# Kernel optimization log

Hardware: AMD Instinct MI355X
Metric: run time of the kernel (lower is better)

The kernel has to match this reference:

```python
import jax, jax.numpy as jnp
import numpy as np

DIM = 768
NUM_HEADS = 12
HEAD_DIM = DIM // NUM_HEADS
SCALE = HEAD_DIM ** -0.5


def setup_inputs() -> dict:
    key = jax.random.key(0)
    ks = jax.random.split(key, 8)
    B, Nx, Ny = 4, 1024, 2048
    std = DIM ** -0.5
    return {
        "x": jax.random.normal(ks[0], (B, Nx, DIM), dtype=jnp.float32),
        "y": jax.random.normal(ks[1], (B, Ny, DIM), dtype=jnp.float32),
        "Wq": jax.random.normal(ks[2], (DIM, DIM), dtype=jnp.float32) * std,
        "Wk": jax.random.normal(ks[3], (DIM, DIM), dtype=jnp.float32) * std,
        "Wv": jax.random.normal(ks[4], (DIM, DIM), dtype=jnp.float32) * std,
        "Wproj": jax.random.normal(ks[5], (DIM, DIM), dtype=jnp.float32) * std,
        "bproj": jnp.zeros((DIM,), dtype=jnp.float32),
    }


def reference(x, y, Wq, Wk, Wv, Wproj, bproj):
    B, Nx, C = x.shape
    Ny = y.shape[1]
    H, D = NUM_HEADS, HEAD_DIM
    # Linear projections (torch nn.Linear: x @ W.T), then split heads -> [B,H,N,D]
    q = (x @ Wq.T).reshape(B, Nx, H, D).transpose(0, 2, 1, 3)
    k = (y @ Wk.T).reshape(B, Ny, H, D).transpose(0, 2, 1, 3)
    v = (y @ Wv.T).reshape(B, Ny, H, D).transpose(0, 2, 1, 3)
    # Manual attention: full [B,H,Nx,Ny] score matrix (faithful to source)
    attn = jnp.einsum("bhqd,bhkd->bhqk", q, k) * SCALE
    attn = jax.nn.softmax(attn, axis=-1)
    out = jnp.einsum("bhqk,bhkd->bhqd", attn, v)
    out = out.transpose(0, 2, 1, 3).reshape(B, Nx, C)
    return out @ Wproj.T + bproj
```

## Files before the change

kernel.cpp:

```cpp
#include <hip/hip_runtime.h>
#include <hip/hip_bf16.h>

typedef unsigned short u16;
typedef __attribute__((ext_vector_type(8))) short bf16x8;
typedef __attribute__((ext_vector_type(4))) float f32x4;
typedef __attribute__((ext_vector_type(16))) float f32x16;
typedef __attribute__((ext_vector_type(4))) unsigned u32x4;

#define MFMA(a, b, c) __builtin_amdgcn_mfma_f32_16x16x32_bf16(a, b, c, 0, 0, 0)
#define MFMA32(a, b, c) __builtin_amdgcn_mfma_f32_32x32x16_bf16(a, b, c, 0, 0, 0)

#define STAGE16(g, l) __builtin_amdgcn_global_load_lds( \
    (const __attribute__((address_space(1))) void*)(g),  \
    (__attribute__((address_space(3))) void*)(l), 16, 0, 0)

#define EXP2(x) __builtin_amdgcn_exp2f(x)

__device__ __forceinline__ u16 f2bf(float f) {
  union { float f; unsigned u; } v; v.f = f;
  return (u16)((v.u + 0x7fffu + ((v.u >> 16) & 1u)) >> 16);
}

__device__ __forceinline__ unsigned pack_bf2(float lo, float hi) {
  unsigned r;
  asm("v_cvt_pk_bf16_f32 %0, %1, %2" : "=v"(r) : "v"(lo), "v"(hi));
  return r;
}

__device__ __forceinline__ void pl32swap(unsigned &a, unsigned &b) {
  asm("v_permlane32_swap_b32 %0, %1" : "+v"(a), "+v"(b));
}

__global__ __launch_bounds__(256) void convert_all(
    const float* __restrict__ x, const float* __restrict__ y,
    const float* __restrict__ wq, const float* __restrict__ wk,
    const float* __restrict__ wv, const float* __restrict__ wp,
    u16* __restrict__ xb, u16* __restrict__ yb,
    u16* __restrict__ wqb, u16* __restrict__ wkb,
    u16* __restrict__ wvb, u16* __restrict__ wpb)
{
  constexpr int G0 = 4096 * 768 / 4;
  constexpr int G1 = G0 + 8192 * 768 / 4;
  constexpr int GW = 768 * 768 / 4;
  int g = blockIdx.x * 256 + threadIdx.x;
  const float* s; u16* d; int o;
  if      (g < G0)          { s = x;  d = xb;  o = g; }
  else if (g < G1)          { s = y;  d = yb;  o = g - G0; }
  else if (g < G1 + GW)     { s = wq; d = wqb; o = g - G1; }
  else if (g < G1 + 2*GW)   { s = wk; d = wkb; o = g - G1 - GW; }
  else if (g < G1 + 3*GW)   { s = wv; d = wvb; o = g - G1 - 2*GW; }
  else if (g < G1 + 4*GW)   { s = wp; d = wpb; o = g - G1 - 3*GW; }
  else return;
  float4 v = reinterpret_cast<const float4*>(s)[o];
  ushort4 r;
  r.x = f2bf(v.x); r.y = f2bf(v.y); r.z = f2bf(v.z); r.w = f2bf(v.w);
  reinterpret_cast<ushort4*>(d)[o] = r;
}

template <bool PROJ>
__global__ __launch_bounds__(256) void gemm_k(
    const u16* __restrict__ A0, const u16* __restrict__ A1,
    const u16* __restrict__ W0, const u16* __restrict__ W1,
    const u16* __restrict__ W2,
    u16* __restrict__ Qa, u16* __restrict__ Ka, u16* __restrict__ Vw,
    const float* __restrict__ bias, float* __restrict__ fout)
{
  __shared__ u16 sA[128 * 64];
  __shared__ u16 sB[128 * 64];

  const int nper = PROJ ? 24 : 120;
  int bid = (blockIdx.x & 7) * nper + (blockIdx.x >> 3);

  const u16 *A, *W;
  int mode, mt, nt;
  if (PROJ)           { mode = 3; A = A0; W = W0; mt = bid / 6;        nt = bid % 6; }
  else if (bid < 192) { mode = 0; A = A0; W = W0; mt = bid / 6;        nt = bid % 6; }
  else if (bid < 576) { mode = 1; A = A1; W = W1; mt = (bid-192) / 6;  nt = (bid-192) % 6; }
  else                { mode = 2; A = A1; W = W2; mt = (bid-576) / 6;  nt = (bid-576) % 6; }

  const int tid = threadIdx.x;
  const int w = tid >> 6, l = tid & 63;
  const int wm = w >> 1, wn = w & 1;
  const int g = l >> 4, m = l & 15;

  const int mbase = mt * 128, nbase = nt * 128;

  const int srow = l >> 3;
  const int schunk = ((l & 7) ^ srow) * 8;
  const u16* Ag = A + (size_t)(mbase + srow) * 768 + schunk;
  const u16* Wg = W + (size_t)(nbase + srow) * 768 + schunk;

  f32x4 acc[4][4] = {};

  for (int kt = 0; kt < 12; ++kt) {
    __syncthreads();
    const int ko = kt * 64;
#pragma unroll
    for (int i = 0; i < 4; ++i) {
      const int ri = (i * 4 + w) * 8;
      STAGE16(Ag + (size_t)ri * 768 + ko, (char*)sA + ri * 128);
      STAGE16(Wg + (size_t)ri * 768 + ko, (char*)sB + ri * 128);
    }
    __syncthreads();

    bf16x8 af[2][4], bfr[2][4];
#pragma unroll
    for (int c = 0; c < 2; ++c)
#pragma unroll
      for (int t = 0; t < 4; ++t) {
        const int ar = wm * 64 + t * 16 + m;
        const int br = wn * 64 + t * 16 + m;
        const int cp = ((c * 4 + g) ^ (l & 7)) * 16;
        af[c][t]  = *reinterpret_cast<const bf16x8*>((const char*)sA + ar * 128 + cp);
        bfr[c][t] = *reinterpret_cast<const bf16x8*>((const char*)sB + br * 128 + cp);
      }
#pragma unroll
    for (int c = 0; c < 2; ++c)
#pragma unroll
      for (int mi = 0; mi < 4; ++mi)
#pragma unroll
        for (int ni = 0; ni < 4; ++ni)
          acc[mi][ni] = MFMA(af[c][mi], bfr[c][ni], acc[mi][ni]);
  }

  const float QSCALE = 0.18033688011112042f;
  const int rowb = mbase + wm * 64 + g * 4;
  const int colb = nbase + wn * 64 + m;
#pragma unroll
  for (int mi = 0; mi < 4; ++mi) {
#pragma unroll
    for (int ni = 0; ni < 4; ++ni) {
      const int col = colb + ni * 16;
      const int h = col >> 6, d = col & 63;
      const int t_ = d >> 4, hh = (d >> 3) & 1, di = d & 7;
      const int fo = t_ * 512 + hh * 256 + di;
      if constexpr (PROJ) {
#pragma unroll
        for (int r = 0; r < 4; ++r) {
          const int row = rowb + mi * 16 + r;
          fout[(size_t)row * 768 + col] = acc[mi][ni][r] + bias[col];
        }
      } else {
        if (mode == 0) {
#pragma unroll
          for (int r = 0; r < 4; ++r) {
            const int row = rowb + mi * 16 + r;
            const int b_ = row >> 10, n = row & 1023;
            Qa[((size_t)(b_ * 12 + h) * 32 + (n >> 5)) * 2048 + fo + (n & 31) * 8] =
                f2bf(acc[mi][ni][r] * QSCALE);
          }
        } else if (mode == 1) {
#pragma unroll
          for (int r = 0; r < 4; ++r) {
            const int row = rowb + mi * 16 + r;
            const int b_ = row >> 11, n = row & 2047;
            Ka[(size_t)(b_ * 12 + h) * 131072 + (n >> 5) * 2048 + fo + (n & 31) * 8] =
                f2bf(acc[mi][ni][r]);
          }
        } else {
          const int row = rowb + mi * 16;
          const int b_ = row >> 11, n = row & 2047;
          ushort4 pk;
          pk.x = f2bf(acc[mi][ni][0]); pk.y = f2bf(acc[mi][ni][1]);
          pk.z = f2bf(acc[mi][ni][2]); pk.w = f2bf(acc[mi][ni][3]);
          *reinterpret_cast<ushort4*>(
              Vw + (size_t)(b_ * 12 + h) * 131072 + (n >> 3) * 512 + d * 8 + (n & 7)) = pk;
        }
      }
    }
  }
}

__global__ __launch_bounds__(128, 3) void attn_fwd(
    const u16* __restrict__ Qa, const u16* __restrict__ Ka,
    const u16* __restrict__ Vw, u16* __restrict__ AOb)
{
  __shared__ float cO[32 * 64];
  __shared__ float cL[32];

  const int bid = blockIdx.x;
  const int bh = bid % 48, qt = bid / 48;
  const int tid = threadIdx.x;
  const int w = tid >> 6, l = tid & 63;
  const int h = l >> 5, q = l & 31;

  const u16* qb = Qa + (size_t)(bh * 32 + qt) * 2048 + h * 256 + q * 8;
  bf16x8 qf[4];
#pragma unroll
  for (int t = 0; t < 4; ++t)
    qf[t] = *reinterpret_cast<const bf16x8*>(qb + t * 512);

  const u16* kb = Ka + (size_t)bh * 131072 + (size_t)w * 65536 + h * 256 + q * 8;
  const u16* vb = Vw + (size_t)bh * 131072 + (size_t)w * 65536 + h * 512 + q * 8;

  bf16x8 ones;
#pragma unroll
  for (int i = 0; i < 8; ++i) ones[i] = (short)0x3F80;

  f32x16 o0 = {}, o1 = {}, la = {};

  for (int kt = 0; kt < 16; ++kt) {
    const u16* kp = kb + kt * 4096;
    const u16* vp = vb + kt * 4096;

    bf16x8 kf0[4], kf1[4];
#pragma unroll
    for (int t = 0; t < 4; ++t) {
      kf0[t] = *reinterpret_cast<const bf16x8*>(kp + t * 512);
      kf1[t] = *reinterpret_cast<const bf16x8*>(kp + 2048 + t * 512);
    }

    f32x16 s0 = {}, s1 = {};
    __builtin_amdgcn_s_setprio(1);
#pragma unroll
    for (int t = 0; t < 4; ++t) {
      s0 = MFMA32(kf0[t], qf[t], s0);
      s1 = MFMA32(kf1[t], qf[t], s1);
    }
    __builtin_amdgcn_s_setprio(0);

    bf16x8 vf0[4], vf1[4];
#pragma unroll
    for (int t = 0; t < 4; ++t) {
      vf0[t] = *reinterpret_cast<const bf16x8*>(vp + t * 1024);
      vf1[t] = *reinterpret_cast<const bf16x8*>(vp + t * 1024 + 256);
    }

    float p0[16], p1[16];
#pragma unroll
    for (int r = 0; r < 16; ++r) p0[r] = EXP2(s0[r]);
#pragma unroll
    for (int r = 0; r < 16; ++r) p1[r] = EXP2(s1[r]);

    unsigned pk[2][4][2];
#pragma unroll
    for (int qd = 0; qd < 4; ++qd) {
      pk[0][qd][0] = pack_bf2(p0[4*qd+0], p0[4*qd+1]);
      pk[0][qd][1] = pack_bf2(p0[4*qd+2], p0[4*qd+3]);
      pk[1][qd][0] = pack_bf2(p1[4*qd+0], p1[4*qd+1]);
      pk[1][qd][1] = pack_bf2(p1[4*qd+2], p1[4*qd+3]);
    }

    __builtin_amdgcn_s_setprio(1);
#pragma unroll
    for (int t = 0; t < 4; ++t) {
      const int c = t >> 1, j0 = 2 * (t & 1);
      unsigned x0 = pk[c][j0][0], y0 = pk[c][j0 + 1][0];
      unsigned x1 = pk[c][j0][1], y1 = pk[c][j0 + 1][1];
      pl32swap(x0, y0);
      pl32swap(x1, y1);
      u32x4 fv; fv[0] = x0; fv[1] = x1; fv[2] = y0; fv[3] = y1;
      const bf16x8 af = __builtin_bit_cast(bf16x8, fv);
      o0 = MFMA32(af, vf0[t], o0);
      o1 = MFMA32(af, vf1[t], o1);
      la = MFMA32(af, ones, la);
    }
    __builtin_amdgcn_s_setprio(0);
  }

  if (w == 1) {
#pragma unroll
    for (int r = 0; r < 16; ++r) {
      const int crow = (r >> 2) * 8 + 4 * h + (r & 3);
      cO[crow * 64 + q]      = o0[r];
      cO[crow * 64 + 32 + q] = o1[r];
      if (q == 0) cL[crow] = la[r];
    }
  }
  __syncthreads();
  if (w == 0) {
    const int b_ = bh / 12, hd = bh % 12;
#pragma unroll
    for (int r = 0; r < 16; ++r) {
      const int crow = (r >> 2) * 8 + 4 * h + (r & 3);
      const float lt = la[r] + cL[crow];
      const float rl = 1.f / lt;
      const float ot0 = o0[r] + cO[crow * 64 + q];
      const float ot1 = o1[r] + cO[crow * 64 + 32 + q];
      u16* dst = AOb + ((size_t)b_ * 1024 + qt * 32 + crow) * 768 + hd * 64 + q;
      dst[0]  = f2bf(ot0 * rl);
      dst[32] = f2bf(ot1 * rl);
    }
  }
}

extern "C" void kernel_launch(void* const* d_in, const int* in_sizes, int n_in,
                              void* d_out, int out_size, void* d_ws, size_t ws_size,
                              hipStream_t stream)
{
  const float* x  = (const float*)d_in[0];
  const float* y  = (const float*)d_in[1];
  const float* wq = (const float*)d_in[2];
  const float* wk = (const float*)d_in[3];
  const float* wv = (const float*)d_in[4];
  const float* wp = (const float*)d_in[5];
  const float* bp = (const float*)d_in[6];
  float* out = (float*)d_out;

  char* ws = (char*)d_ws;
  u16* xb  = (u16*)ws; ws += (size_t)4096 * 768 * 2;
  u16* yb  = (u16*)ws; ws += (size_t)8192 * 768 * 2;
  u16* wqb = (u16*)ws; ws += (size_t)768 * 768 * 2;
  u16* wkb = (u16*)ws; ws += (size_t)768 * 768 * 2;
  u16* wvb = (u16*)ws; ws += (size_t)768 * 768 * 2;
  u16* wpb = (u16*)ws; ws += (size_t)768 * 768 * 2;
  u16* Qa  = (u16*)ws; ws += (size_t)4096 * 768 * 2;
  u16* Ka  = (u16*)ws; ws += (size_t)8192 * 768 * 2;
  u16* Vw  = (u16*)ws; ws += (size_t)8192 * 768 * 2;
  u16* AOb = (u16*)ws; ws += (size_t)4096 * 768 * 2;

  convert_all<<<11520, 256, 0, stream>>>(x, y, wq, wk, wv, wp,
                                         xb, yb, wqb, wkb, wvb, wpb);
  gemm_k<false><<<960, 256, 0, stream>>>(xb, yb, wqb, wkb, wvb,
                                         Qa, Ka, Vw, nullptr, nullptr);
  attn_fwd<<<1536, 128, 0, stream>>>(Qa, Ka, Vw, AOb);
  gemm_k<true><<<192, 256, 0, stream>>>(AOb, nullptr, wpb, nullptr, nullptr,
                                        nullptr, nullptr, nullptr, bp, out);
}
```

Measured before the change: 110.8 us.

## Double-buffer GEMM LDS tiles and share K/V tiles across attention waves

The GEMM kernel gains a two-stage LDS double buffer so the next k-tile's global-to-LDS copy is issued before computing on the current one, replacing two barriers per step with one. The attention kernel is restructured so each 256-thread block holds four waves, each owning its own 32-row query tile, and all four share K/V tiles staged cooperatively into double-buffered LDS. Previously two waves split the key range and each read K/V directly from global memory. The row-sum is now computed with VALU adds and a shuffle instead of an extra MFMA against ones, which also removes the cross-wave LDS reduction. The cost is fewer blocks (384) and more LDS per block, which may limit occupancy.

Result: slower. 120.1 us (+8.4%).

```diff
diff --git a/kernel.cpp b/kernel.cpp
--- a/kernel.cpp
+++ b/kernel.cpp
@@ -65,8 +65,8 @@
     u16* __restrict__ Qa, u16* __restrict__ Ka, u16* __restrict__ Vw,
     const float* __restrict__ bias, float* __restrict__ fout)
 {
-  __shared__ u16 sA[128 * 64];
-  __shared__ u16 sB[128 * 64];
+  __shared__ u16 sA[2][128 * 64];
+  __shared__ u16 sB[2][128 * 64];
 
   const int nper = PROJ ? 24 : 120;
   int bid = (blockIdx.x & 7) * nper + (blockIdx.x >> 3);
@@ -92,17 +92,28 @@
 
   f32x4 acc[4][4] = {};
 
+#pragma unroll
+  for (int i = 0; i < 4; ++i) {
+    const int ri = (i * 4 + w) * 8;
+    STAGE16(Ag + (size_t)ri * 768, (char*)sA[0] + ri * 128);
+    STAGE16(Wg + (size_t)ri * 768, (char*)sB[0] + ri * 128);
+  }
+
   for (int kt = 0; kt < 12; ++kt) {
     __syncthreads();
-    const int ko = kt * 64;
-#pragma unroll
-    for (int i = 0; i < 4; ++i) {
-      const int ri = (i * 4 + w) * 8;
-      STAGE16(Ag + (size_t)ri * 768 + ko, (char*)sA + ri * 128);
-      STAGE16(Wg + (size_t)ri * 768 + ko, (char*)sB + ri * 128);
-    }
-    __syncthreads();
-
+
+    if (kt < 11) {
+      const int ko = (kt + 1) * 64;
+      const int nb = (kt + 1) & 1;
+#pragma unroll
+      for (int i = 0; i < 4; ++i) {
+        const int ri = (i * 4 + w) * 8;
+        STAGE16(Ag + (size_t)ri * 768 + ko, (char*)sA[nb] + ri * 128);
+        STAGE16(Wg + (size_t)ri * 768 + ko, (char*)sB[nb] + ri * 128);
+      }
+    }
+
+    const int cb = kt & 1;
     bf16x8 af[2][4], bfr[2][4];
 #pragma unroll
     for (int c = 0; c < 2; ++c)
@@ -111,8 +122,8 @@
         const int ar = wm * 64 + t * 16 + m;
         const int br = wn * 64 + t * 16 + m;
         const int cp = ((c * 4 + g) ^ (l & 7)) * 16;
-        af[c][t]  = *reinterpret_cast<const bf16x8*>((const char*)sA + ar * 128 + cp);
-        bfr[c][t] = *reinterpret_cast<const bf16x8*>((const char*)sB + br * 128 + cp);
+        af[c][t]  = *reinterpret_cast<const bf16x8*>((const char*)sA[cb] + ar * 128 + cp);
+        bfr[c][t] = *reinterpret_cast<const bf16x8*>((const char*)sB[cb] + br * 128 + cp);
       }
 #pragma unroll
     for (int c = 0; c < 2; ++c)
@@ -171,12 +182,12 @@
   }
 }
 
-__global__ __launch_bounds__(128, 3) void attn_fwd(
+__global__ __launch_bounds__(256, 4) void attn_fwd(
     const u16* __restrict__ Qa, const u16* __restrict__ Ka,
     const u16* __restrict__ Vw, u16* __restrict__ AOb)
 {
-  __shared__ float cO[32 * 64];
-  __shared__ float cL[32];
+  __shared__ u16 sK[2][4096];
+  __shared__ u16 sV[2][4096];
 
   const int bid = blockIdx.x;
   const int bh = bid % 48, qt = bid / 48;
@@ -184,30 +195,49 @@
   const int w = tid >> 6, l = tid & 63;
   const int h = l >> 5, q = l & 31;
 
-  const u16* qb = Qa + (size_t)(bh * 32 + qt) * 2048 + h * 256 + q * 8;
+  const u16* qb = Qa + (size_t)(bh * 32 + qt * 4 + w) * 2048 + h * 256 + q * 8;
   bf16x8 qf[4];
 #pragma unroll
   for (int t = 0; t < 4; ++t)
     qf[t] = *reinterpret_cast<const bf16x8*>(qb + t * 512);
 
-  const u16* kb = Ka + (size_t)bh * 131072 + (size_t)w * 65536 + h * 256 + q * 8;
-  const u16* vb = Vw + (size_t)bh * 131072 + (size_t)w * 65536 + h * 512 + q * 8;
-
-  bf16x8 ones;
-#pragma unroll
-  for (int i = 0; i < 8; ++i) ones[i] = (short)0x3F80;
-
-  f32x16 o0 = {}, o1 = {}, la = {};
-
-  for (int kt = 0; kt < 16; ++kt) {
-    const u16* kp = kb + kt * 4096;
-    const u16* vp = vb + kt * 4096;
+  const u16* Kbh = Ka + (size_t)bh * 131072;
+  const u16* Vbh = Vw + (size_t)bh * 131072;
+
+  const int sbase = w * 1024;
+  const u16* Ksrc = Kbh + sbase + l * 8;
+  const u16* Vsrc = Vbh + sbase + l * 8;
+
+  f32x16 o0 = {}, o1 = {};
+  float lrun = 0.f;
+
+#pragma unroll
+  for (int i = 0; i < 2; ++i) {
+    STAGE16(Ksrc + i * 512, (char*)&sK[0][sbase + i * 512]);
+    STAGE16(Vsrc + i * 512, (char*)&sV[0][sbase + i * 512]);
+  }
+
+  for (int kt = 0; kt < 32; ++kt) {
+    __syncthreads();
+
+    if (kt < 31) {
+      const int nb = (kt + 1) & 1;
+      const size_t go = (size_t)(kt + 1) * 4096;
+#pragma unroll
+      for (int i = 0; i < 2; ++i) {
+        STAGE16(Ksrc + go + i * 512, (char*)&sK[nb][sbase + i * 512]);
+        STAGE16(Vsrc + go + i * 512, (char*)&sV[nb][sbase + i * 512]);
+      }
+    }
+
+    const u16* kp = &sK[kt & 1][0];
+    const u16* vp = &sV[kt & 1][0];
 
     bf16x8 kf0[4], kf1[4];
 #pragma unroll
     for (int t = 0; t < 4; ++t) {
-      kf0[t] = *reinterpret_cast<const bf16x8*>(kp + t * 512);
-      kf1[t] = *reinterpret_cast<const bf16x8*>(kp + 2048 + t * 512);
+      kf0[t] = *reinterpret_cast<const bf16x8*>(kp + t * 512 + h * 256 + q * 8);
+      kf1[t] = *reinterpret_cast<const bf16x8*>(kp + 2048 + t * 512 + h * 256 + q * 8);
     }
 
     f32x16 s0 = {}, s1 = {};
@@ -222,8 +252,8 @@
     bf16x8 vf0[4], vf1[4];
 #pragma unroll
     for (int t = 0; t < 4; ++t) {
-      vf0[t] = *reinterpret_cast<const bf16x8*>(vp + t * 1024);
-      vf1[t] = *reinterpret_cast<const bf16x8*>(vp + t * 1024 + 256);
+      vf0[t] = *reinterpret_cast<const bf16x8*>(vp + t * 1024 + h * 512 + q * 8);
+      vf1[t] = *reinterpret_cast<const bf16x8*>(vp + t * 1024 + h * 512 + q * 8 + 256);
     }
 
     float p0[16], p1[16];
@@ -231,6 +261,12 @@
     for (int r = 0; r < 16; ++r) p0[r] = EXP2(s0[r]);
 #pragma unroll
     for (int r = 0; r < 16; ++r) p1[r] = EXP2(s1[r]);
+
+    float a8[8];
+#pragma unroll
+    for (int i = 0; i < 8; ++i)
+      a8[i] = (p0[2*i] + p0[2*i+1]) + (p1[2*i] + p1[2*i+1]);
+    lrun += ((a8[0]+a8[1]) + (a8[2]+a8[3])) + ((a8[4]+a8[5]) + (a8[6]+a8[7]));
 
     unsigned pk[2][4][2];
 #pragma unroll
@@ -253,34 +289,20 @@
       const bf16x8 af = __builtin_bit_cast(bf16x8, fv);
       o0 = MFMA32(af, vf0[t], o0);
       o1 = MFMA32(af, vf1[t], o1);
-      la = MFMA32(af, ones, la);
     }
     __builtin_amdgcn_s_setprio(0);
   }
 
-  if (w == 1) {
-#pragma unroll
-    for (int r = 0; r < 16; ++r) {
-      const int crow = (r >> 2) * 8 + 4 * h + (r & 3);
-      cO[crow * 64 + q]      = o0[r];
-      cO[crow * 64 + 32 + q] = o1[r];
-      if (q == 0) cL[crow] = la[r];
-    }
-  }
-  __syncthreads();
-  if (w == 0) {
-    const int b_ = bh / 12, hd = bh % 12;
-#pragma unroll
-    for (int r = 0; r < 16; ++r) {
-      const int crow = (r >> 2) * 8 + 4 * h + (r & 3);
-      const float lt = la[r] + cL[crow];
-      const float rl = 1.f / lt;
-      const float ot0 = o0[r] + cO[crow * 64 + q];
-      const float ot1 = o1[r] + cO[crow * 64 + 32 + q];
-      u16* dst = AOb + ((size_t)b_ * 1024 + qt * 32 + crow) * 768 + hd * 64 + q;
-      dst[0]  = f2bf(ot0 * rl);
-      dst[32] = f2bf(ot1 * rl);
-    }
+  lrun += __shfl_xor(lrun, 32);
+  const int b_ = bh / 12, hd = bh % 12;
+  const int q0 = (qt * 4 + w) * 32;
+#pragma unroll
+  for (int r = 0; r < 16; ++r) {
+    const int crow = (r >> 2) * 8 + 4 * h + (r & 3);
+    const float rl = 1.f / __shfl(lrun, crow);
+    u16* dst = AOb + ((size_t)b_ * 1024 + q0 + crow) * 768 + hd * 64 + q;
+    dst[0]  = f2bf(o0[r] * rl);
+    dst[32] = f2bf(o1[r] * rl);
   }
 }
 
@@ -313,7 +335,7 @@
                                          xb, yb, wqb, wkb, wvb, wpb);
   gemm_k<false><<<960, 256, 0, stream>>>(xb, yb, wqb, wkb, wvb,
                                          Qa, Ka, Vw, nullptr, nullptr);
-  attn_fwd<<<1536, 128, 0, stream>>>(Qa, Ka, Vw, AOb);
+  attn_fwd<<<384, 256, 0, stream>>>(Qa, Ka, Vw, AOb);
   gemm_k<true><<<192, 256, 0, stream>>>(AOb, nullptr, wpb, nullptr, nullptr,
                                         nullptr, nullptr, nullptr, bp, out);
 }
```
